# Kernel optimization log

Measured on AMD Instinct MI355X. Metric: run time of the kernel, lower is better.

The kernel has to match this reference:

```python
import jax, jax.numpy as jnp
import numpy as np

ADAPTERS = 40   # adapter_num, hard-coded by range(40) and tsv 40x40
CAPS = 3        # num_capsules
CLASS_DIM = 200 # MAX_SEQ
IN_CH = CAPS * CLASS_DIM  # 600
B = 256
D = 768
NUM_ITERS = 3


def squash(v, axis=-1):
    sq = jnp.sum(v * v, axis=axis, keepdims=True)
    return (sq / (1.0 + sq)) * v / jnp.sqrt(sq)


def setup_inputs() -> dict:
    key = jax.random.key(0)
    k0, k1, k2, k3, k4 = jax.random.split(key, 5)
    x = jax.random.normal(k0, (B, ADAPTERS, IN_CH), jnp.float32)
    s = jax.random.uniform(k1, (1,), jnp.float32) * 4.0 + 1.0  # gate temperature
    route_weights = jax.random.normal(k2, (ADAPTERS, CAPS, IN_CH, CLASS_DIM), jnp.float32)
    larger_w = jax.random.normal(k3, (D, CAPS), jnp.float32) * 0.1  # Linear(3,768) weight [out,in]
    larger_b = jnp.zeros((D,), jnp.float32)
    elarger = jax.random.normal(k4, (ADAPTERS, D), jnp.float32)     # Embedding(40,768)
    tsv = jnp.tril(jnp.ones((ADAPTERS, ADAPTERS), jnp.float32))
    return {"t": 20, "x": x, "s": s, "route_weights": route_weights,
            "larger_w": larger_w, "larger_b": larger_b, "elarger": elarger, "tsv": tsv}


def reference(t, x, s, route_weights, larger_w, larger_b, elarger, tsv):
    bz = x.shape[0]
    # per-adapter small matmuls, batched: priors[n,b,k,d] = sum_c x[b,k,c] * W[k,n,c,d]
    priors = jnp.einsum('bkc,kncd->nbkd', x, route_weights)[:, :, :, None, :]  # [3,B,40,1,200]
    tsv_t = tsv[t]                                   # [40]
    mask = jnp.where(tsv_t == 0, -10000.0, 0.0)      # [40]
    tsv_b = tsv_t[None, None, :, None, None]
    mask_b = mask[None, None, :, None, None]
    logits = jnp.zeros_like(priors)
    vote = None
    for i in range(NUM_ITERS):
        logits = logits * tsv_b + mask_b
        probs = jax.nn.softmax(logits, axis=2)       # my_softmax over adapter dim
        vote = jnp.sum(probs * priors, axis=2, keepdims=True)   # [3,B,1,1,200]
        out = squash(vote, axis=-1)
        if i != NUM_ITERS - 1:
            logits = logits + jnp.sum(priors * out, axis=-1, keepdims=True)
    # torch's .view(bz, length, -1) on a [3,B,1,1,200] tensor: row-major reinterpretation
    h = vote.reshape(bz, CLASS_DIM, CAPS)            # [B,200,3]
    h = h @ larger_w.T + larger_b                    # [B,200,768]
    g = jax.nn.sigmoid(s * elarger[t])               # [768] (broadcast of [1]*[768])
    return h * g
```

## Files before the change

### kernel.cpp

```cpp
#include <hip/hip_runtime.h>
#include <hip/hip_bf16.h>

#define ADAPTERS 40
#define CAPS 3
#define IN_CH 600
#define BSZ 256
#define DCLS 200
#define DMODEL 768

typedef __attribute__((ext_vector_type(8))) short short8;
typedef __attribute__((ext_vector_type(4))) float f32x4;

__global__ void k0_gw(const float* __restrict__ s_p,
                      const float* __restrict__ lw,
                      const float* __restrict__ lb,
                      const float* __restrict__ el,
                      const int* __restrict__ t_p,
                      float4* __restrict__ gw4) {
    int j = blockIdx.x * blockDim.x + threadIdx.x;
    if (j >= DMODEL) return;
    float s = s_p[0];
    int t = t_p[0];
    float e = el[t * DMODEL + j];
    float g = 1.0f / (1.0f + expf(-s * e));
    gw4[j] = make_float4(g * lw[j * 3 + 0], g * lw[j * 3 + 1],
                         g * lw[j * 3 + 2], g * lb[j]);
}

#define RP 40
#define NCHUNK 19

__device__ __forceinline__ void split2(float f0, float f1,
                                       unsigned& hi, unsigned& lo) {
    unsigned u0 = __float_as_uint(f0), u1 = __float_as_uint(f1);
    unsigned h0 = u0 & 0xFFFF0000u, h1 = u1 & 0xFFFF0000u;
    hi = (u0 >> 16) | h1;
    float l0 = f0 - __uint_as_float(h0);
    float l1 = f1 - __uint_as_float(h1);
    lo = (__float_as_uint(l0) >> 16) | (__float_as_uint(l1) & 0xFFFF0000u);
}

__global__ __launch_bounds__(256) void k1_priors(
    const float* __restrict__ x,
    const float* __restrict__ rw,
    const float* __restrict__ tsv,
    const int* __restrict__ t_p,
    float* __restrict__ priors)
{
    int kk = blockIdx.z;
    int t = t_p[0];
    if (tsv[t * ADAPTERS + kk] == 0.0f) return;

    int b0 = blockIdx.x * 128;
    int j0 = blockIdx.y * 128;

    __shared__ __align__(16) unsigned short Ahi[128 * RP];
    __shared__ __align__(16) unsigned short Alo[128 * RP];
    __shared__ __align__(16) unsigned short Bhi[128 * RP];
    __shared__ __align__(16) unsigned short Blo[128 * RP];

    int tid = threadIdx.x;
    int lane = tid & 63, w = tid >> 6;
    int lm = lane & 15, lq = lane >> 4;
    int m0w = (w & 1) * 64, n0w = (w >> 1) * 64;

    int a_bi = tid >> 1;
    int a_ci0 = (tid & 1) * 16;
    const float* a_row = x + ((size_t)(b0 + a_bi) * ADAPTERS + kk) * IN_CH;
    int b_jj = tid >> 1;
    int b_ci0 = (tid & 1) * 16;
    int j = j0 + b_jj;
    bool jvalid = (j < CAPS * DCLS);
    int cap = (j >= 2 * DCLS) ? 2 : ((j >= DCLS) ? 1 : 0);
    int d = j - cap * DCLS;
    const float* b_base = rw + ((size_t)(kk * 3 + cap) * IN_CH) * DCLS + d;

    f32x4 acc[4][4];
    #pragma unroll
    for (int mt = 0; mt < 4; mt++)
        #pragma unroll
        for (int nt = 0; nt < 4; nt++)
            acc[mt][nt] = (f32x4){0.f, 0.f, 0.f, 0.f};

    float4 ax[4];
    float  bx[16];

    {
        int c0 = 0;
        #pragma unroll
        for (int q = 0; q < 4; q++) {
            int c = c0 + a_ci0 + q * 4;
            ax[q] = (c + 4 <= IN_CH) ? *(const float4*)(a_row + c)
                                     : make_float4(0.f, 0.f, 0.f, 0.f);
        }
        #pragma unroll
        for (int i = 0; i < 16; i++) {
            int c = c0 + b_ci0 + i;
            bx[i] = (jvalid && c < IN_CH) ? b_base[(size_t)c * DCLS] : 0.f;
        }
    }

    for (int ch = 0; ch < NCHUNK; ch++) {
        unsigned ahi[8], alo[8], bhi[8], blo[8];
        #pragma unroll
        for (int q = 0; q < 4; q++) {
            split2(ax[q].x, ax[q].y, ahi[q * 2], alo[q * 2]);
            split2(ax[q].z, ax[q].w, ahi[q * 2 + 1], alo[q * 2 + 1]);
        }
        #pragma unroll
        for (int p = 0; p < 8; p++)
            split2(bx[2 * p], bx[2 * p + 1], bhi[p], blo[p]);

        __syncthreads();
        {
            unsigned* pa = (unsigned*)&Ahi[a_bi * RP + a_ci0];
            *(uint4*)pa = make_uint4(ahi[0], ahi[1], ahi[2], ahi[3]);
            *(uint4*)(pa + 4) = make_uint4(ahi[4], ahi[5], ahi[6], ahi[7]);
            unsigned* pl = (unsigned*)&Alo[a_bi * RP + a_ci0];
            *(uint4*)pl = make_uint4(alo[0], alo[1], alo[2], alo[3]);
            *(uint4*)(pl + 4) = make_uint4(alo[4], alo[5], alo[6], alo[7]);
            unsigned* pb = (unsigned*)&Bhi[b_jj * RP + b_ci0];
            *(uint4*)pb = make_uint4(bhi[0], bhi[1], bhi[2], bhi[3]);
            *(uint4*)(pb + 4) = make_uint4(bhi[4], bhi[5], bhi[6], bhi[7]);
            unsigned* pc = (unsigned*)&Blo[b_jj * RP + b_ci0];
            *(uint4*)pc = make_uint4(blo[0], blo[1], blo[2], blo[3]);
            *(uint4*)(pc + 4) = make_uint4(blo[4], blo[5], blo[6], blo[7]);
        }
        __syncthreads();

        if (ch + 1 < NCHUNK) {
            int c0 = (ch + 1) * 32;
            #pragma unroll
            for (int q = 0; q < 4; q++) {
                int c = c0 + a_ci0 + q * 4;
                ax[q] = (c + 4 <= IN_CH) ? *(const float4*)(a_row + c)
                                         : make_float4(0.f, 0.f, 0.f, 0.f);
            }
            #pragma unroll
            for (int i = 0; i < 16; i++) {
                int c = c0 + b_ci0 + i;
                bx[i] = (jvalid && c < IN_CH) ? b_base[(size_t)c * DCLS] : 0.f;
            }
        }

        short8 Afh[4], Afl[4];
        #pragma unroll
        for (int mt = 0; mt < 4; mt++) {
            int row = m0w + mt * 16 + lm;
            Afh[mt] = *(const short8*)&Ahi[row * RP + lq * 8];
            Afl[mt] = *(const short8*)&Alo[row * RP + lq * 8];
        }
        #pragma unroll
        for (int nt = 0; nt < 4; nt++) {
            int row = n0w + nt * 16 + lm;
            short8 bh = *(const short8*)&Bhi[row * RP + lq * 8];
            short8 bl = *(const short8*)&Blo[row * RP + lq * 8];
            #pragma unroll
            for (int mt = 0; mt < 4; mt++) {
                acc[mt][nt] = __builtin_amdgcn_mfma_f32_16x16x32_bf16(
                    Afh[mt], bh, acc[mt][nt], 0, 0, 0);
                acc[mt][nt] = __builtin_amdgcn_mfma_f32_16x16x32_bf16(
                    Afh[mt], bl, acc[mt][nt], 0, 0, 0);
                acc[mt][nt] = __builtin_amdgcn_mfma_f32_16x16x32_bf16(
                    Afl[mt], bh, acc[mt][nt], 0, 0, 0);
            }
        }
    }

    #pragma unroll
    for (int nt = 0; nt < 4; nt++) {
        int jc = j0 + n0w + nt * 16 + lm;
        if (jc >= CAPS * DCLS) continue;
        int capc = (jc >= 2 * DCLS) ? 2 : ((jc >= DCLS) ? 1 : 0);
        int dc = jc - capc * DCLS;
        #pragma unroll
        for (int mt = 0; mt < 4; mt++) {
            int bbase = b0 + m0w + mt * 16 + lq * 4;
            #pragma unroll
            for (int r = 0; r < 4; r++) {
                int b = bbase + r;
                priors[((size_t)(capc * BSZ + b) * ADAPTERS + kk) * DCLS + dc] =
                    acc[mt][nt][r];
            }
        }
    }
}

__global__ __launch_bounds__(256) void k2_route(
    const float* __restrict__ priors,
    const float* __restrict__ tsv,
    const int* __restrict__ t_p,
    float* __restrict__ vote)
{
    int nb = blockIdx.x;
    int n = nb >> 8, b = nb & 255;
    int tid = threadIdx.x;
    int lane = tid & 63, wid = tid >> 6;

    __shared__ float Ps[ADAPTERS * DCLS];
    __shared__ float vout[DCLS];
    __shared__ float a_s[ADAPTERS];
    __shared__ float probs_s[ADAPTERS];
    __shared__ float act[ADAPTERS];
    __shared__ float red[4];
    __shared__ float scl;

    int t = t_p[0];
    if (tid < ADAPTERS) {
        act[tid] = tsv[t * ADAPTERS + tid];
        a_s[tid] = 0.0f;
    }
    __syncthreads();

    const float* pb = priors + (size_t)(n * BSZ + b) * ADAPTERS * DCLS;
    for (int idx = tid; idx < ADAPTERS * DCLS; idx += 256) {
        int k = idx / DCLS;
        if (act[k] != 0.0f) Ps[idx] = pb[idx];
    }
    __syncthreads();

    float cnt = 0.0f;
    for (int k = 0; k < ADAPTERS; k++) cnt += (act[k] != 0.f) ? 1.f : 0.f;

    int td = tid;
    float v = 0.0f;
    if (td < DCLS) {
        for (int k = 0; k < ADAPTERS; k++)
            if (act[k] != 0.f) v += Ps[k * DCLS + td];
        v /= cnt;
    }

    for (int it = 0; it < 3; it++) {
        if (it > 0) {
            if (wid == 0) {
                bool on = (lane < ADAPTERS) && (act[lane] != 0.f);
                float val = on ? a_s[lane] : -3.0e38f;
                float m = val;
                for (int off = 32; off; off >>= 1)
                    m = fmaxf(m, __shfl_down(m, off));
                m = __shfl(m, 0);
                float e = on ? expf(val - m) : 0.f;
                float ssum = e;
                for (int off = 32; off; off >>= 1)
                    ssum += __shfl_down(ssum, off);
                ssum = __shfl(ssum, 0);
                if (lane < ADAPTERS) probs_s[lane] = e / ssum;
            }
            __syncthreads();
            v = 0.0f;
            if (td < DCLS) {
                for (int k = 0; k < ADAPTERS; k++)
                    if (act[k] != 0.f) v += probs_s[k] * Ps[k * DCLS + td];
            }
        }
        if (it == 2) break;

        float vv = (td < DCLS) ? v * v : 0.f;
        for (int off = 32; off; off >>= 1) vv += __shfl_down(vv, off);
        if (lane == 0) red[wid] = vv;
        __syncthreads();
        if (tid == 0) {
            float sq = red[0] + red[1] + red[2] + red[3];
            scl = sqrtf(sq) / (1.0f + sq);
        }
        __syncthreads();
        if (td < DCLS) vout[td] = v * scl;
        __syncthreads();

        for (int k = wid; k < ADAPTERS; k += 4) {
            if (act[k] == 0.f) continue;
            const float* row = Ps + k * DCLS;
            float p = row[lane] * vout[lane]
                    + row[lane + 64] * vout[lane + 64]
                    + row[lane + 128] * vout[lane + 128];
            if (lane < DCLS - 192) p += row[lane + 192] * vout[lane + 192];
            for (int off = 32; off; off >>= 1) p += __shfl_down(p, off);
            if (lane == 0) a_s[k] += p;
        }
        __syncthreads();
    }

    if (td < DCLS) vote[(size_t)n * BSZ * DCLS + b * DCLS + td] = v;
}

typedef __attribute__((ext_vector_type(4))) float f4v;

__global__ __launch_bounds__(256) void k3_out(
    const float* __restrict__ vote,
    const float4* __restrict__ gw4,
    float* __restrict__ out)
{
    __shared__ float vs[192];
    int tid = threadIdx.x;
    int r0 = blockIdx.x * 64;
    if (tid < 192) vs[tid] = vote[r0 * 3 + tid];
    __syncthreads();

    int lane = tid & 63;
    int ty = tid >> 6;
    int j = blockIdx.y * 256 + lane * 4;

    float4 g0 = gw4[j + 0];
    float4 g1 = gw4[j + 1];
    float4 g2 = gw4[j + 2];
    float4 g3 = gw4[j + 3];

    #pragma unroll
    for (int it = 0; it < 16; it++) {
        int rl = it * 4 + ty;
        float h0 = vs[rl * 3 + 0];
        float h1 = vs[rl * 3 + 1];
        float h2 = vs[rl * 3 + 2];
        f4v o;
        o.x = h0 * g0.x + h1 * g0.y + h2 * g0.z + g0.w;
        o.y = h0 * g1.x + h1 * g1.y + h2 * g1.z + g1.w;
        o.z = h0 * g2.x + h1 * g2.y + h2 * g2.z + g2.w;
        o.w = h0 * g3.x + h1 * g3.y + h2 * g3.z + g3.w;
        __builtin_nontemporal_store(o, (f4v*)(out + (size_t)(r0 + rl) * DMODEL + j));
    }
}

extern "C" void kernel_launch(void* const* d_in, const int* in_sizes, int n_in,
                              void* d_out, int out_size, void* d_ws, size_t ws_size,
                              hipStream_t stream) {
    const int*   t   = (const int*)d_in[0];
    const float* x   = (const float*)d_in[1];
    const float* s   = (const float*)d_in[2];
    const float* rw  = (const float*)d_in[3];
    const float* lw  = (const float*)d_in[4];
    const float* lb  = (const float*)d_in[5];
    const float* el  = (const float*)d_in[6];
    const float* tsv = (const float*)d_in[7];
    float* out = (float*)d_out;

    char* wsb = (char*)d_ws;
    float*  priors = (float*)wsb;
    float*  vote   = (float*)(wsb + 24576000);
    float4* gw4    = (float4*)(wsb + 25190400);

    k0_gw<<<dim3(3), dim3(256), 0, stream>>>(s, lw, lb, el, t, gw4);
    k1_priors<<<dim3(2, 5, ADAPTERS), dim3(256), 0, stream>>>(x, rw, tsv, t, priors);
    k2_route<<<dim3(CAPS * BSZ), dim3(256), 0, stream>>>(priors, tsv, t, vote);
    k3_out<<<dim3(BSZ * DCLS / 64, 3), dim3(256), 0, stream>>>(vote, gw4, out);
}
```

Measured before the change: 298.3 us.

## Fuse routing and output projection into one kernel with register prefetch

Merges the gate-weight, routing and output-projection kernels into a single kernel where each block handles three consecutive (n,b) rows of the flattened vote tensor. Each block routes those three rows in sequence and then writes the resulting 200x768 output slice directly. The next prior slice is prefetched into registers while the current one is routed, and the gate weights are recomputed per block instead of in a separate launch. This removes two launches and the vote/gw4 round trip through global memory. The costs are 256 blocks instead of 768, which lowers parallelism, plus higher register pressure from the 32-entry prefetch array.

```diff
diff --git a/kernel.cpp b/kernel.cpp
--- a/kernel.cpp
+++ b/kernel.cpp
@@ -10,22 +10,7 @@
 
 typedef __attribute__((ext_vector_type(8))) short short8;
 typedef __attribute__((ext_vector_type(4))) float f32x4;
-
-__global__ void k0_gw(const float* __restrict__ s_p,
-                      const float* __restrict__ lw,
-                      const float* __restrict__ lb,
-                      const float* __restrict__ el,
-                      const int* __restrict__ t_p,
-                      float4* __restrict__ gw4) {
-    int j = blockIdx.x * blockDim.x + threadIdx.x;
-    if (j >= DMODEL) return;
-    float s = s_p[0];
-    int t = t_p[0];
-    float e = el[t * DMODEL + j];
-    float g = 1.0f / (1.0f + expf(-s * e));
-    gw4[j] = make_float4(g * lw[j * 3 + 0], g * lw[j * 3 + 1],
-                         g * lw[j * 3 + 2], g * lb[j]);
-}
+typedef __attribute__((ext_vector_type(4))) float f4v;
 
 #define RP 40
 #define NCHUNK 19
@@ -186,137 +171,154 @@
     }
 }
 
-__global__ __launch_bounds__(256) void k2_route(
+#define NPRE 32
+
+__global__ __launch_bounds__(256) void k23_fused(
     const float* __restrict__ priors,
     const float* __restrict__ tsv,
     const int* __restrict__ t_p,
-    float* __restrict__ vote)
+    const float* __restrict__ s_p,
+    const float* __restrict__ lw,
+    const float* __restrict__ lb,
+    const float* __restrict__ el,
+    float* __restrict__ out)
 {
-    int nb = blockIdx.x;
-    int n = nb >> 8, b = nb & 255;
+    int b2 = blockIdx.x;
     int tid = threadIdx.x;
     int lane = tid & 63, wid = tid >> 6;
 
     __shared__ float Ps[ADAPTERS * DCLS];
+    __shared__ float vloc[3 * DCLS];
     __shared__ float vout[DCLS];
+    __shared__ float act[ADAPTERS];
     __shared__ float a_s[ADAPTERS];
     __shared__ float probs_s[ADAPTERS];
-    __shared__ float act[ADAPTERS];
     __shared__ float red[4];
     __shared__ float scl;
 
     int t = t_p[0];
-    if (tid < ADAPTERS) {
-        act[tid] = tsv[t * ADAPTERS + tid];
-        a_s[tid] = 0.0f;
-    }
-    __syncthreads();
-
-    const float* pb = priors + (size_t)(n * BSZ + b) * ADAPTERS * DCLS;
-    for (int idx = tid; idx < ADAPTERS * DCLS; idx += 256) {
-        int k = idx / DCLS;
-        if (act[k] != 0.0f) Ps[idx] = pb[idx];
-    }
+    if (tid < ADAPTERS) act[tid] = tsv[t * ADAPTERS + tid];
     __syncthreads();
 
     float cnt = 0.0f;
     for (int k = 0; k < ADAPTERS; k++) cnt += (act[k] != 0.f) ? 1.f : 0.f;
 
-    int td = tid;
-    float v = 0.0f;
-    if (td < DCLS) {
-        for (int k = 0; k < ADAPTERS; k++)
-            if (act[k] != 0.f) v += Ps[k * DCLS + td];
-        v /= cnt;
-    }
-
-    for (int it = 0; it < 3; it++) {
-        if (it > 0) {
-            if (wid == 0) {
-                bool on = (lane < ADAPTERS) && (act[lane] != 0.f);
-                float val = on ? a_s[lane] : -3.0e38f;
-                float m = val;
-                for (int off = 32; off; off >>= 1)
-                    m = fmaxf(m, __shfl_down(m, off));
-                m = __shfl(m, 0);
-                float e = on ? expf(val - m) : 0.f;
-                float ssum = e;
-                for (int off = 32; off; off >>= 1)
-                    ssum += __shfl_down(ssum, off);
-                ssum = __shfl(ssum, 0);
-                if (lane < ADAPTERS) probs_s[lane] = e / ssum;
-            }
+    float4 gj[4];
+    if (tid < DMODEL / 4) {
+        float s = s_p[0];
+        #pragma unroll
+        for (int jj = 0; jj < 4; jj++) {
+            int j = tid * 4 + jj;
+            float e = el[t * DMODEL + j];
+            float g = 1.0f / (1.0f + expf(-s * e));
+            gj[jj] = make_float4(g * lw[j * 3 + 0], g * lw[j * 3 + 1],
+                                 g * lw[j * 3 + 2], g * lb[j]);
+        }
+    }
+
+    float pre[NPRE];
+    #pragma unroll
+    for (int i = 0; i < NPRE; i++) pre[i] = 0.0f;
+
+    auto prefetch = [&](int q) {
+        const float* p = priors + (size_t)q * (ADAPTERS * DCLS);
+        #pragma unroll
+        for (int i = 0; i < NPRE; i++) {
+            int idx = i * 256 + tid;
+            if (idx < ADAPTERS * DCLS) {
+                int k = idx / DCLS;
+                if (act[k] != 0.f) pre[i] = p[idx];
+            }
+        }
+    };
+    prefetch(3 * b2);
+
+    for (int qi = 0; qi < 3; qi++) {
+        #pragma unroll
+        for (int i = 0; i < NPRE; i++) {
+            int idx = i * 256 + tid;
+            if (idx < ADAPTERS * DCLS) Ps[idx] = pre[i];
+        }
+        if (tid < ADAPTERS) a_s[tid] = 0.0f;
+        __syncthreads();
+        if (qi < 2) prefetch(3 * b2 + qi + 1);
+
+        int td = tid;
+        float v = 0.0f;
+        if (td < DCLS) {
+            for (int k = 0; k < ADAPTERS; k++)
+                if (act[k] != 0.f) v += Ps[k * DCLS + td];
+            v /= cnt;
+        }
+
+        for (int it = 0; it < 3; it++) {
+            if (it > 0) {
+                if (wid == 0) {
+                    bool on = (lane < ADAPTERS) && (act[lane] != 0.f);
+                    float val = on ? a_s[lane] : -3.0e38f;
+                    float m = val;
+                    for (int off = 32; off; off >>= 1)
+                        m = fmaxf(m, __shfl_down(m, off));
+                    m = __shfl(m, 0);
+                    float e = on ? expf(val - m) : 0.f;
+                    float ssum = e;
+                    for (int off = 32; off; off >>= 1)
+                        ssum += __shfl_down(ssum, off);
+                    ssum = __shfl(ssum, 0);
+                    if (lane < ADAPTERS) probs_s[lane] = e / ssum;
+                }
+                __syncthreads();
+                v = 0.0f;
+                if (td < DCLS) {
+                    for (int k = 0; k < ADAPTERS; k++)
+                        if (act[k] != 0.f) v += probs_s[k] * Ps[k * DCLS + td];
+                }
+            }
+            if (it == 2) break;
+
+            float vv = (td < DCLS) ? v * v : 0.f;
+            for (int off = 32; off; off >>= 1) vv += __shfl_down(vv, off);
+            if (lane == 0) red[wid] = vv;
             __syncthreads();
-            v = 0.0f;
-            if (td < DCLS) {
-                for (int k = 0; k < ADAPTERS; k++)
-                    if (act[k] != 0.f) v += probs_s[k] * Ps[k * DCLS + td];
-            }
-        }
-        if (it == 2) break;
-
-        float vv = (td < DCLS) ? v * v : 0.f;
-        for (int off = 32; off; off >>= 1) vv += __shfl_down(vv, off);
-        if (lane == 0) red[wid] = vv;
+            if (tid == 0) {
+                float sq = red[0] + red[1] + red[2] + red[3];
+                scl = sqrtf(sq) / (1.0f + sq);
+            }
+            __syncthreads();
+            if (td < DCLS) vout[td] = v * scl;
+            __syncthreads();
+
+            for (int k = wid; k < ADAPTERS; k += 4) {
+                if (act[k] == 0.f) continue;
+                const float* row = Ps + k * DCLS;
+                float p = row[lane] * vout[lane]
+                        + row[lane + 64] * vout[lane + 64]
+                        + row[lane + 128] * vout[lane + 128];
+                if (lane < DCLS - 192) p += row[lane + 192] * vout[lane + 192];
+                for (int off = 32; off; off >>= 1) p += __shfl_down(p, off);
+                if (lane == 0) a_s[k] += p;
+            }
+            __syncthreads();
+        }
+
+        if (td < DCLS) vloc[qi * DCLS + td] = v;
         __syncthreads();
-        if (tid == 0) {
-            float sq = red[0] + red[1] + red[2] + red[3];
-            scl = sqrtf(sq) / (1.0f + sq);
-        }
-        __syncthreads();
-        if (td < DCLS) vout[td] = v * scl;
-        __syncthreads();
-
-        for (int k = wid; k < ADAPTERS; k += 4) {
-            if (act[k] == 0.f) continue;
-            const float* row = Ps + k * DCLS;
-            float p = row[lane] * vout[lane]
-                    + row[lane + 64] * vout[lane + 64]
-                    + row[lane + 128] * vout[lane + 128];
-            if (lane < DCLS - 192) p += row[lane + 192] * vout[lane + 192];
-            for (int off = 32; off; off >>= 1) p += __shfl_down(p, off);
-            if (lane == 0) a_s[k] += p;
-        }
-        __syncthreads();
-    }
-
-    if (td < DCLS) vote[(size_t)n * BSZ * DCLS + b * DCLS + td] = v;
-}
-
-typedef __attribute__((ext_vector_type(4))) float f4v;
-
-__global__ __launch_bounds__(256) void k3_out(
-    const float* __restrict__ vote,
-    const float4* __restrict__ gw4,
-    float* __restrict__ out)
-{
-    __shared__ float vs[192];
-    int tid = threadIdx.x;
-    int r0 = blockIdx.x * 64;
-    if (tid < 192) vs[tid] = vote[r0 * 3 + tid];
-    __syncthreads();
-
-    int lane = tid & 63;
-    int ty = tid >> 6;
-    int j = blockIdx.y * 256 + lane * 4;
-
-    float4 g0 = gw4[j + 0];
-    float4 g1 = gw4[j + 1];
-    float4 g2 = gw4[j + 2];
-    float4 g3 = gw4[j + 3];
-
-    #pragma unroll
-    for (int it = 0; it < 16; it++) {
-        int rl = it * 4 + ty;
-        float h0 = vs[rl * 3 + 0];
-        float h1 = vs[rl * 3 + 1];
-        float h2 = vs[rl * 3 + 2];
-        f4v o;
-        o.x = h0 * g0.x + h1 * g0.y + h2 * g0.z + g0.w;
-        o.y = h0 * g1.x + h1 * g1.y + h2 * g1.z + g1.w;
-        o.z = h0 * g2.x + h1 * g2.y + h2 * g2.z + g2.w;
-        o.w = h0 * g3.x + h1 * g3.y + h2 * g3.z + g3.w;
-        __builtin_nontemporal_store(o, (f4v*)(out + (size_t)(r0 + rl) * DMODEL + j));
+    }
+
+    if (tid < DMODEL / 4) {
+        float* rowp = out + (size_t)b2 * DCLS * DMODEL + tid * 4;
+        #pragma unroll 4
+        for (int r = 0; r < DCLS; r++) {
+            float h0 = vloc[r * 3 + 0];
+            float h1 = vloc[r * 3 + 1];
+            float h2 = vloc[r * 3 + 2];
+            f4v o;
+            o.x = h0 * gj[0].x + h1 * gj[0].y + h2 * gj[0].z + gj[0].w;
+            o.y = h0 * gj[1].x + h1 * gj[1].y + h2 * gj[1].z + gj[1].w;
+            o.z = h0 * gj[2].x + h1 * gj[2].y + h2 * gj[2].z + gj[2].w;
+            o.w = h0 * gj[3].x + h1 * gj[3].y + h2 * gj[3].z + gj[3].w;
+            __builtin_nontemporal_store(o, (f4v*)(rowp + (size_t)r * DMODEL));
+        }
     }
 }
 
@@ -333,13 +335,8 @@
     const float* tsv = (const float*)d_in[7];
     float* out = (float*)d_out;
 
-    char* wsb = (char*)d_ws;
-    float*  priors = (float*)wsb;
-    float*  vote   = (float*)(wsb + 24576000);
-    float4* gw4    = (float4*)(wsb + 25190400);
-
-    k0_gw<<<dim3(3), dim3(256), 0, stream>>>(s, lw, lb, el, t, gw4);
+    float* priors = (float*)d_ws;
+
     k1_priors<<<dim3(2, 5, ADAPTERS), dim3(256), 0, stream>>>(x, rw, tsv, t, priors);
-    k2_route<<<dim3(CAPS * BSZ), dim3(256), 0, stream>>>(priors, tsv, t, vote);
-    k3_out<<<dim3(BSZ * DCLS / 64, 3), dim3(256), 0, stream>>>(vote, gw4, out);
+    k23_fused<<<dim3(BSZ), dim3(256), 0, stream>>>(priors, tsv, t, s, lw, lb, el, out);
 }
```

Result: slower. 318.5 us (+6.8%).

## Transpose MFMA operands for vectorized prior stores and compact active adapter list

Applied to the files above, without the earlier changes.

The MFMA operands are swapped so each lane's accumulator holds four consecutive class-dim values. Priors can then be written as one float4 store instead of four scattered scalar stores. The routing kernel loads priors into shared memory with float4 loads and builds a compacted list of active adapters, so the loops no longer branch on the mask for every adapter. Correctness relies on dc being 4-aligned and not straddling capsule boundaries, which holds because 200 is divisible by 4.

```diff
diff --git a/kernel.cpp b/kernel.cpp
--- a/kernel.cpp
+++ b/kernel.cpp
@@ -10,6 +10,7 @@
 
 typedef __attribute__((ext_vector_type(8))) short short8;
 typedef __attribute__((ext_vector_type(4))) float f32x4;
+typedef __attribute__((ext_vector_type(4))) float f4v;
 
 __global__ void k0_gw(const float* __restrict__ s_p,
                       const float* __restrict__ lw,
@@ -158,30 +159,27 @@
             #pragma unroll
             for (int mt = 0; mt < 4; mt++) {
                 acc[mt][nt] = __builtin_amdgcn_mfma_f32_16x16x32_bf16(
-                    Afh[mt], bh, acc[mt][nt], 0, 0, 0);
+                    bh, Afh[mt], acc[mt][nt], 0, 0, 0);
                 acc[mt][nt] = __builtin_amdgcn_mfma_f32_16x16x32_bf16(
-                    Afh[mt], bl, acc[mt][nt], 0, 0, 0);
+                    bl, Afh[mt], acc[mt][nt], 0, 0, 0);
                 acc[mt][nt] = __builtin_amdgcn_mfma_f32_16x16x32_bf16(
-                    Afl[mt], bh, acc[mt][nt], 0, 0, 0);
+                    bh, Afl[mt], acc[mt][nt], 0, 0, 0);
             }
         }
     }
 
     #pragma unroll
     for (int nt = 0; nt < 4; nt++) {
-        int jc = j0 + n0w + nt * 16 + lm;
+        int jc = j0 + n0w + nt * 16 + lq * 4;
         if (jc >= CAPS * DCLS) continue;
         int capc = (jc >= 2 * DCLS) ? 2 : ((jc >= DCLS) ? 1 : 0);
         int dc = jc - capc * DCLS;
         #pragma unroll
         for (int mt = 0; mt < 4; mt++) {
-            int bbase = b0 + m0w + mt * 16 + lq * 4;
-            #pragma unroll
-            for (int r = 0; r < 4; r++) {
-                int b = bbase + r;
-                priors[((size_t)(capc * BSZ + b) * ADAPTERS + kk) * DCLS + dc] =
-                    acc[mt][nt][r];
-            }
+            int b = b0 + m0w + mt * 16 + lm;
+            float* dst = priors +
+                ((size_t)(capc * BSZ + b) * ADAPTERS + kk) * DCLS + dc;
+            *(f4v*)dst = *(f4v*)&acc[mt][nt];
         }
     }
 }
@@ -199,9 +197,11 @@
 
     __shared__ float Ps[ADAPTERS * DCLS];
     __shared__ float vout[DCLS];
+    __shared__ float act[ADAPTERS];
     __shared__ float a_s[ADAPTERS];
     __shared__ float probs_s[ADAPTERS];
-    __shared__ float act[ADAPTERS];
+    __shared__ int   klist[ADAPTERS];
+    __shared__ int   nact_s;
     __shared__ float red[4];
     __shared__ float scl;
 
@@ -212,21 +212,32 @@
     }
     __syncthreads();
 
-    const float* pb = priors + (size_t)(n * BSZ + b) * ADAPTERS * DCLS;
-    for (int idx = tid; idx < ADAPTERS * DCLS; idx += 256) {
-        int k = idx / DCLS;
-        if (act[k] != 0.0f) Ps[idx] = pb[idx];
+    if (tid == 0) {
+        int c = 0;
+        for (int k = 0; k < ADAPTERS; k++)
+            if (act[k] != 0.0f) klist[c++] = k;
+        nact_s = c;
+    }
+
+    {
+        const float4* pb4 = (const float4*)
+            (priors + (size_t)(n * BSZ + b) * ADAPTERS * DCLS);
+        float4* Ps4 = (float4*)Ps;
+        for (int i4 = tid; i4 < ADAPTERS * (DCLS / 4); i4 += 256) {
+            int k = i4 / (DCLS / 4);
+            if (act[k] != 0.0f) Ps4[i4] = pb4[i4];
+        }
     }
     __syncthreads();
 
-    float cnt = 0.0f;
-    for (int k = 0; k < ADAPTERS; k++) cnt += (act[k] != 0.f) ? 1.f : 0.f;
+    int nact = nact_s;
+    float cnt = (float)nact;
 
     int td = tid;
     float v = 0.0f;
     if (td < DCLS) {
-        for (int k = 0; k < ADAPTERS; k++)
-            if (act[k] != 0.f) v += Ps[k * DCLS + td];
+        for (int ki = 0; ki < nact; ki++)
+            v += Ps[klist[ki] * DCLS + td];
         v /= cnt;
     }
 
@@ -249,8 +260,10 @@
             __syncthreads();
             v = 0.0f;
             if (td < DCLS) {
-                for (int k = 0; k < ADAPTERS; k++)
-                    if (act[k] != 0.f) v += probs_s[k] * Ps[k * DCLS + td];
+                for (int ki = 0; ki < nact; ki++) {
+                    int k = klist[ki];
+                    v += probs_s[k] * Ps[k * DCLS + td];
+                }
             }
         }
         if (it == 2) break;
@@ -267,8 +280,8 @@
         if (td < DCLS) vout[td] = v * scl;
         __syncthreads();
 
-        for (int k = wid; k < ADAPTERS; k += 4) {
-            if (act[k] == 0.f) continue;
+        for (int ki = wid; ki < nact; ki += 4) {
+            int k = klist[ki];
             const float* row = Ps + k * DCLS;
             float p = row[lane] * vout[lane]
                     + row[lane + 64] * vout[lane + 64]
@@ -282,8 +295,6 @@
 
     if (td < DCLS) vote[(size_t)n * BSZ * DCLS + b * DCLS + td] = v;
 }
-
-typedef __attribute__((ext_vector_type(4))) float f4v;
 
 __global__ __launch_bounds__(256) void k3_out(
     const float* __restrict__ vote,
```

Measured after the change: 292.4 us. Within noise of the previous version (-2.0%).
